# Kernel optimization log

Hardware: AMD Instinct MI355X
Metric: run time of the kernel (lower is better)

## Reference

```python
import jax, jax.numpy as jnp
import numpy as np

IN_FEATURES = 8192
OUT_FEATURES = 28672
BATCH = 8  # tokens; skinny GEMM -> memory-bound weight streaming


def setup_inputs() -> dict:
    key = jax.random.key(0)
    k1, k2, k3, k4 = jax.random.split(key, 4)
    x = jax.random.normal(k1, (BATCH, IN_FEATURES), dtype=jnp.float32)
    # ternary codes in {0,1,2} -> weight values {-1,0,+1}; pack 4 codes / byte
    codes = jax.random.randint(k2, (OUT_FEATURES, IN_FEATURES), 0, 3, dtype=jnp.int32)
    codes4 = codes.reshape(OUT_FEATURES, IN_FEATURES // 4, 4)
    shifts = jnp.array([0, 2, 4, 6], dtype=jnp.int32)
    packed_weight = jnp.sum(codes4 << shifts, axis=-1).astype(jnp.int32)  # [O, I//4]
    weight_scale = jax.random.uniform(k3, (1,), dtype=jnp.float32, minval=0.01, maxval=0.1)
    bias = jax.random.normal(k4, (OUT_FEATURES,), dtype=jnp.float32)
    return {"x": x, "packed_weight": packed_weight, "weight_scale": weight_scale, "bias": bias}


def _unpack_ternary(packed):
    # [O, I//4] int -> [O, I] ternary in {-1,0,1}
    shifts = jnp.array([0, 2, 4, 6], dtype=jnp.int32)
    w = ((packed[:, :, None] >> shifts) & 3) - 1  # [O, I//4, 4]
    return w.reshape(packed.shape[0], -1)


def reference(x, packed_weight, weight_scale, bias):
    B = x.shape[0]
    x_flat = x.reshape(B, IN_FEATURES)
    # per-tensor absmax int8 activation quantization
    absmax = jnp.maximum(jnp.max(jnp.abs(x_flat)), 1e-5)
    act_scale = absmax / 127.0
    x_q = jnp.clip(jnp.round(x_flat / act_scale), -128, 127)  # int8 values, kept f32
    w = _unpack_ternary(packed_weight).astype(jnp.float32)  # [O, I]
    # fused dequant GEMM: integer-valued accumulation, single scalar scale
    acc = jnp.einsum('bi,oi->bo', x_q, w)  # exact in f32 (|acc| << 2^24)
    scale = weight_scale[0] * act_scale
    out = acc * scale + bias
    return out.reshape(B, OUT_FEATURES)
```

## Files before the change

kernel.cpp:

```cpp
#include <hip/hip_runtime.h>
#include <stdint.h>

#define O_FEATS 28672
#define I_FEATS 8192
#define BATCH 8
#define WPR 2048

typedef int i32x4 __attribute__((ext_vector_type(4)));


static __device__ __forceinline__ int unpack4(uint32_t p) {
  uint32_t lo = p & 0x0Fu;
  uint32_t hi = (p >> 4) & 0x0Fu;
  uint32_t a = (lo * 0x41u) & 0x0303u;
  uint32_t b = (hi * 0x41u) & 0x0303u;
  return (int)(a | (b << 16));
}

__global__ void k_absmax(const float* __restrict__ x, uint32_t* __restrict__ ws) {
  __shared__ float red[4];
  int t = threadIdx.x;
  float4 v = ((const float4*)x)[blockIdx.x * 256 + t];
  float m = fmaxf(fmaxf(fabsf(v.x), fabsf(v.y)), fmaxf(fabsf(v.z), fabsf(v.w)));
#pragma unroll
  for (int off = 32; off; off >>= 1)
    m = fmaxf(m, __shfl_xor(m, off));
  if ((t & 63) == 0) red[t >> 6] = m;
  __syncthreads();
  if (t == 0)
    ws[16 + blockIdx.x] =
        __float_as_uint(fmaxf(fmaxf(red[0], red[1]), fmaxf(red[2], red[3])));
}

__global__ void k_quant(const float* __restrict__ x, uint32_t* __restrict__ ws) {
  __shared__ float s_amax;
  __shared__ int reds[4];
  int t = threadIdx.x;
  if (blockIdx.x >= 64) {
    int row = 8 + ((blockIdx.x - 64) >> 3), seg = blockIdx.x & 7;
    ws[1024 + row * 2048 + seg * 256 + t] = 0u;
    return;
  }
  int b = blockIdx.x >> 3, seg = blockIdx.x & 7;
  if (t < 64) {
    float m = __uint_as_float(ws[16 + t]);
#pragma unroll
    for (int off = 32; off; off >>= 1)
      m = fmaxf(m, __shfl_xor(m, off));
    if (t == 0) {
      float a = fmaxf(m, 1e-5f);
      s_amax = a;
      ws[0] = __float_as_uint(a);
    }
  }
  __syncthreads();
  float s = s_amax / 127.0f;
  float4 v = ((const float4*)(x + b * I_FEATS + seg * 1024))[t];
  int q0 = (int)fminf(fmaxf(rintf(v.x / s), -128.f), 127.f);
  int q1 = (int)fminf(fmaxf(rintf(v.y / s), -128.f), 127.f);
  int q2 = (int)fminf(fmaxf(rintf(v.z / s), -128.f), 127.f);
  int q3 = (int)fminf(fmaxf(rintf(v.w / s), -128.f), 127.f);
  uint32_t pk = (uint32_t)(q0 & 0xff) | ((uint32_t)(q1 & 0xff) << 8) |
                ((uint32_t)(q2 & 0xff) << 16) | ((uint32_t)(q3 & 0xff) << 24);
  ws[1024 + b * 2048 + seg * 256 + t] = pk;
  int s4 = q0 + q1 + q2 + q3;
#pragma unroll
  for (int off = 32; off; off >>= 1)
    s4 += __shfl_xor(s4, off);
  if ((t & 63) == 0) reds[t >> 6] = s4;
  __syncthreads();
  if (t == 0)
    ws[128 + blockIdx.x] = (uint32_t)(reds[0] + reds[1] + reds[2] + reds[3]);
}

__global__ void __launch_bounds__(256, 4)
k_gemm(const int* __restrict__ Wp, const float* __restrict__ wscale,
       const float* __restrict__ bias, const uint32_t* __restrict__ ws,
       float* __restrict__ out) {
  __shared__ int red[4][32][4];
  __shared__ int s_sumx[BATCH];
  __shared__ float s_scale;

  const int t = threadIdx.x;
  const int wave = t >> 6, lane = t & 63;

  if (t < 64) {
    int p = (int)ws[128 + t];
    p += __shfl_xor(p, 1);
    p += __shfl_xor(p, 2);
    p += __shfl_xor(p, 4);
    if ((t & 7) == 0) s_sumx[t >> 3] = p;
    if (t == 0) s_scale = (__uint_as_float(ws[0]) / 127.0f) * wscale[0];
  }

  const int tile = blockIdx.x * 2 + (wave >> 1);
  const int khalf = wave & 1;
  const int o_base = tile * 16;
  const int m = lane & 15, g = lane >> 4;

  const uint8_t* xq8 = (const uint8_t*)(ws + 1024);
  const int4* ap = (const int4*)(xq8 + m * 8192 + khalf * 4096 + g * 16);
  const int4* wp =
      (const int4*)((const uint8_t*)Wp + (o_base + m) * 8192 + khalf * 4096 + g * 16);

  i32x4 acc = {0, 0, 0, 0};
  int4 a0 = ap[0], b0 = wp[0];
#pragma unroll 4
  for (int s = 0; s < 64; ++s) {
    int4 a1, b1;
    if (s < 63) {
      a1 = ap[(s + 1) * 4];
      b1 = wp[(s + 1) * 4];
    }
    i32x4 af, bf;
    af.x = a0.x; af.y = a0.y; af.z = a0.z; af.w = a0.w;
    bf.x = unpack4((uint32_t)b0.x);
    bf.y = unpack4((uint32_t)b0.y);
    bf.z = unpack4((uint32_t)b0.z);
    bf.w = unpack4((uint32_t)b0.w);
    acc = __builtin_amdgcn_mfma_i32_16x16x64_i8(af, bf, acc, 0, 0, 0);
    a0 = a1;
    b0 = b1;
  }

  if (lane < 32) {
#pragma unroll
    for (int r = 0; r < 4; ++r) red[wave][lane][r] = acc[r];
  }
  __syncthreads();

  if (khalf == 0 && lane < 32) {
    const int n = lane & 15;
    const int q = lane >> 4;
    const int o = o_base + n;
    const float bo = bias[o];
#pragma unroll
    for (int r = 0; r < 4; ++r) {
      int mm = q * 4 + r;
      int tot = red[wave][lane][r] + red[wave + 1][lane][r];
      out[mm * O_FEATS + o] = (float)(tot - s_sumx[mm]) * s_scale + bo;
    }
  }
}

extern "C" void kernel_launch(void* const* d_in, const int* in_sizes, int n_in,
                              void* d_out, int out_size, void* d_ws, size_t ws_size,
                              hipStream_t stream) {
  const float* x = (const float*)d_in[0];
  const int* pw = (const int*)d_in[1];
  const float* wscale = (const float*)d_in[2];
  const float* bias = (const float*)d_in[3];
  float* out = (float*)d_out;
  uint32_t* ws = (uint32_t*)d_ws;

  k_absmax<<<64, 256, 0, stream>>>(x, ws);
  k_quant<<<128, 256, 0, stream>>>(x, ws);
  k_gemm<<<O_FEATS / 32, 256, 0, stream>>>(pw, wscale, bias, ws, out);
}
```

Before: 344.4 us.

## Split K across four waves per 16-row tile with 4-deep load prefetch

Each block now covers one 16-output tile, with its four waves each taking a quarter of the K dimension instead of two tiles split two ways. The block count doubles. The inner loop now keeps four loads in flight through a fully unrolled ring buffer instead of one-ahead prefetch, and launch bounds rise to 7 blocks per CU. The aim is more memory-level parallelism for weight streaming. The cost is a four-way LDS reduction per tile and possible register pressure from the deeper buffers.

```diff
diff --git a/kernel.cpp b/kernel.cpp
--- a/kernel.cpp
+++ b/kernel.cpp
@@ -4,7 +4,6 @@
 #define O_FEATS 28672
 #define I_FEATS 8192
 #define BATCH 8
-#define WPR 2048
 
 typedef int i32x4 __attribute__((ext_vector_type(4)));
 
@@ -73,7 +72,7 @@
     ws[128 + blockIdx.x] = (uint32_t)(reds[0] + reds[1] + reds[2] + reds[3]);
 }
 
-__global__ void __launch_bounds__(256, 4)
+__global__ void __launch_bounds__(256, 7)
 k_gemm(const int* __restrict__ Wp, const float* __restrict__ wscale,
        const float* __restrict__ bias, const uint32_t* __restrict__ ws,
        float* __restrict__ out) {
@@ -93,34 +92,36 @@
     if (t == 0) s_scale = (__uint_as_float(ws[0]) / 127.0f) * wscale[0];
   }
 
-  const int tile = blockIdx.x * 2 + (wave >> 1);
-  const int khalf = wave & 1;
-  const int o_base = tile * 16;
+  const int o_base = blockIdx.x * 16;
   const int m = lane & 15, g = lane >> 4;
 
   const uint8_t* xq8 = (const uint8_t*)(ws + 1024);
-  const int4* ap = (const int4*)(xq8 + m * 8192 + khalf * 4096 + g * 16);
-  const int4* wp =
-      (const int4*)((const uint8_t*)Wp + (o_base + m) * 8192 + khalf * 4096 + g * 16);
+  const int4* ap = (const int4*)(xq8 + m * 8192 + wave * 2048 + g * 16);
+  const int4* wp = (const int4*)((const uint8_t*)Wp + (size_t)(o_base + m) * 8192 +
+                                 wave * 2048 + g * 16);
 
   i32x4 acc = {0, 0, 0, 0};
-  int4 a0 = ap[0], b0 = wp[0];
-#pragma unroll 4
-  for (int s = 0; s < 64; ++s) {
-    int4 a1, b1;
-    if (s < 63) {
-      a1 = ap[(s + 1) * 4];
-      b1 = wp[(s + 1) * 4];
+  int4 abuf[4], bbuf[4];
+#pragma unroll
+  for (int i = 0; i < 4; ++i) {
+    abuf[i] = ap[i * 4];
+    bbuf[i] = wp[i * 4];
+  }
+#pragma unroll
+  for (int s = 0; s < 32; ++s) {
+    int4 a = abuf[s & 3];
+    int4 b = bbuf[s & 3];
+    if (s + 4 < 32) {
+      abuf[s & 3] = ap[(s + 4) * 4];
+      bbuf[s & 3] = wp[(s + 4) * 4];
     }
     i32x4 af, bf;
-    af.x = a0.x; af.y = a0.y; af.z = a0.z; af.w = a0.w;
-    bf.x = unpack4((uint32_t)b0.x);
-    bf.y = unpack4((uint32_t)b0.y);
-    bf.z = unpack4((uint32_t)b0.z);
-    bf.w = unpack4((uint32_t)b0.w);
+    af.x = a.x; af.y = a.y; af.z = a.z; af.w = a.w;
+    bf.x = unpack4((uint32_t)b.x);
+    bf.y = unpack4((uint32_t)b.y);
+    bf.z = unpack4((uint32_t)b.z);
+    bf.w = unpack4((uint32_t)b.w);
     acc = __builtin_amdgcn_mfma_i32_16x16x64_i8(af, bf, acc, 0, 0, 0);
-    a0 = a1;
-    b0 = b1;
   }
 
   if (lane < 32) {
@@ -129,15 +130,15 @@
   }
   __syncthreads();
 
-  if (khalf == 0 && lane < 32) {
-    const int n = lane & 15;
-    const int q = lane >> 4;
+  if (t < 32) {
+    const int n = t & 15;
+    const int q = t >> 4;
     const int o = o_base + n;
     const float bo = bias[o];
 #pragma unroll
     for (int r = 0; r < 4; ++r) {
       int mm = q * 4 + r;
-      int tot = red[wave][lane][r] + red[wave + 1][lane][r];
+      int tot = red[0][t][r] + red[1][t][r] + red[2][t][r] + red[3][t][r];
       out[mm * O_FEATS + o] = (float)(tot - s_sumx[mm]) * s_scale + bo;
     }
   }
@@ -155,5 +156,5 @@
 
   k_absmax<<<64, 256, 0, stream>>>(x, ws);
   k_quant<<<128, 256, 0, stream>>>(x, ws);
-  k_gemm<<<O_FEATS / 32, 256, 0, stream>>>(pw, wscale, bias, ws, out);
+  k_gemm<<<O_FEATS / 16, 256, 0, stream>>>(pw, wscale, bias, ws, out);
 }
```

After: 334.2 us. 3.0% less time.
